# Kernel tuning notes

Measured on AMD Instinct MI355X. Metric: run time of the kernel, lower is better.

Reference implementation:

```python
import jax, jax.numpy as jnp
import numpy as np

NUM_CLASSES = 80
BATCH_PER_IMG = 512
POS_FRAC = 0.25
IOU_THRESH = 0.5
NUM_FG_TARGET = int(BATCH_PER_IMG * POS_FRAC)  # 128


def _make_boxes(k, shape):
    raw = jax.random.uniform(k, shape + (4,), dtype=jnp.float32)
    x1 = raw[..., 0] * 900.0
    y1 = raw[..., 1] * 900.0
    w = raw[..., 2] * 120.0 + 4.0
    h = raw[..., 3] * 120.0 + 4.0
    return jnp.stack([x1, y1, x1 + w, y1 + h], axis=-1)


def setup_inputs() -> dict:
    B, N, M = 16, 20000, 128
    key = jax.random.key(0)
    k1, k2, k3, k4, k5 = jax.random.split(key, 5)
    gt_boxes = _make_boxes(k1, (B, M))
    proposal_boxes = _make_boxes(k2, (B, N))
    # make the first M proposals jittered copies of gt so some match above IoU 0.5
    jitter = jax.random.normal(k5, (B, M, 4), dtype=jnp.float32) * 3.0
    proposal_boxes = proposal_boxes.at[:, :M, :].set(gt_boxes + jitter)
    gt_classes = jax.random.randint(k3, (B, M), 0, NUM_CLASSES)
    keys = jax.random.uniform(k4, (B, N), dtype=jnp.float32)  # random sampling priorities
    return {"gt_boxes": gt_boxes, "gt_classes": gt_classes,
            "proposal_boxes": proposal_boxes, "keys": keys}


def _pairwise_iou(gt, pr):
    # gt: [M,4], pr: [N,4], xyxy -> [M,N]
    area_g = (gt[:, 2] - gt[:, 0]) * (gt[:, 3] - gt[:, 1])
    area_p = (pr[:, 2] - pr[:, 0]) * (pr[:, 3] - pr[:, 1])
    lt = jnp.maximum(gt[:, None, :2], pr[None, :, :2])
    rb = jnp.minimum(gt[:, None, 2:], pr[None, :, 2:])
    wh = jnp.clip(rb - lt, 0.0)
    inter = wh[..., 0] * wh[..., 1]
    return inter / (area_g[:, None] + area_p[None, :] - inter)


def _per_image(gt_b, gt_c, pr_b, key_f):
    iou = _pairwise_iou(gt_b, pr_b)          # [M,N]
    matched_vals = iou.max(axis=0)           # [N]  (ious in torch code)
    matched_idxs = iou.argmax(axis=0)        # [N]  matcher assignment
    matched_labels = matched_vals >= IOU_THRESH  # thresholds [0.5], labels [0,1]
    cls = jnp.where(matched_labels, gt_c[matched_idxs], NUM_CLASSES)  # bg = num_classes
    fg = cls != NUM_CLASSES
    fg_take = jnp.minimum(NUM_FG_TARGET, fg.sum())  # subsample_labels fg quota
    BIG = jnp.float32(1e9)
    fg_order = jnp.argsort(jnp.where(fg, key_f, BIG))   # random fg subset via random keys
    bg_order = jnp.argsort(jnp.where(fg, BIG, key_f))   # random bg subset
    i = jnp.arange(BATCH_PER_IMG)
    sampled = jnp.where(i < fg_take, fg_order[i], bg_order[jnp.clip(i - fg_take, 0)])
    s_cls = cls[sampled]                         # gt_classes field
    s_iou = matched_vals[sampled]                # proposals.iou field
    s_gt_boxes = gt_b[matched_idxs[sampled]]     # gt_boxes field gather
    float_out = jnp.concatenate([s_iou[:, None], s_gt_boxes], axis=-1)  # [512,5]
    return sampled, s_cls, float_out


def reference(gt_boxes, gt_classes, proposal_boxes, keys):
    sampled_idxs, sampled_classes, float_out = jax.vmap(_per_image)(
        gt_boxes, gt_classes, proposal_boxes, keys)
    return float_out, sampled_classes, sampled_idxs
```

## Files before the change

### kernel.cpp

```cpp
#include <hip/hip_runtime.h>
#include <stdint.h>

constexpr int Bn     = 16;
constexpr int Nn     = 20000;
constexpr int Mn     = 128;
constexpr int NCLS   = 80;
constexpr int BATCH  = 512;
constexpr int FG_TGT = 128;
constexpr float KEY_T = 0.06f;

constexpr int TPB = 256;
constexpr int TPI = (Nn + TPB - 1) / TPB;
constexpr int NT  = Bn * TPI;

typedef unsigned long long u64;

__global__ __launch_bounds__(256) void classify_kernel(
    const float* __restrict__ gt_boxes, const float* __restrict__ prop,
    const float* __restrict__ keys,
    u64* __restrict__ fgsl, u64* __restrict__ bgsl,
    int* __restrict__ fcnt, int* __restrict__ bcnt)
{
    const int t    = blockIdx.x;
    const int b    = t / TPI;
    const int blk  = t % TPI;
    const int tid  = threadIdx.x;
    const int lane = tid & 63;

    __shared__ u64 fgl[256];
    __shared__ u64 bgl[256];
    __shared__ int lcnt[2];
    if (tid < 2) lcnt[tid] = 0;
    __syncthreads();

    const float4 g0 = ((const float4*)gt_boxes)[(size_t)b * Mn + 2 * lane];
    const float4 g1 = ((const float4*)gt_boxes)[(size_t)b * Mn + 2 * lane + 1];
    const float a0 = __fmul_rn(__fsub_rn(g0.z, g0.x), __fsub_rn(g0.w, g0.y));
    const float a1 = __fmul_rn(__fsub_rn(g1.z, g1.x), __fsub_rn(g1.w, g1.y));

    const int n0 = __builtin_amdgcn_readfirstlane(blk * 256 + (tid >> 6) * 64);
    const float4* __restrict__ pp = (const float4*)prop + (size_t)b * Nn + n0;
    u64 fgmask = 0;

#define IOU_BODY(IDX)                                                          \
    {                                                                          \
        const float4 p = pp[IDX];                       \
        const float ap = __fmul_rn(__fsub_rn(p.z, p.x), __fsub_rn(p.w, p.y)); \
        float w0 = fmaxf(__fsub_rn(fminf(g0.z, p.z), fmaxf(g0.x, p.x)), 0.0f);\
        float h0 = fmaxf(__fsub_rn(fminf(g0.w, p.w), fmaxf(g0.y, p.y)), 0.0f);\
        float i0 = __fmul_rn(w0, h0);                                          \
        float d0 = __fsub_rn(__fadd_rn(a0, ap), i0);                           \
        float q0 = __fadd_rn(i0, i0);                                          \
        float t0 = __builtin_fmaf(d0, -0x1p-20f, d0);                          \
        float w1 = fmaxf(__fsub_rn(fminf(g1.z, p.z), fmaxf(g1.x, p.x)), 0.0f);\
        float h1 = fmaxf(__fsub_rn(fminf(g1.w, p.w), fmaxf(g1.y, p.y)), 0.0f);\
        float i1 = __fmul_rn(w1, h1);                                          \
        float d1 = __fsub_rn(__fadd_rn(a1, ap), i1);                           \
        float q1 = __fadd_rn(i1, i1);                                          \
        float t1 = __builtin_fmaf(d1, -0x1p-20f, d1);                          \
        bool ambl = (q0 >= t0) | (q1 >= t1);                                   \
        if (__ballot(ambl) != 0) {                     \
            bool e0 = (2.0 * (double)i0 >= (double)d0 * (1.0 - 0x1p-25));      \
            bool e1 = (2.0 * (double)i1 >= (double)d1 * (1.0 - 0x1p-25));      \
            bool def = __ballot(e0 | e1) != 0;                                 \
            fgmask |= ((u64)(def ? 1 : 0)) << (IDX);                           \
        }                                                                      \
    }

    if (n0 + 64 <= Nn) {
        #pragma unroll 8
        for (int i = 0; i < 64; ++i) IOU_BODY(i)
    } else if (n0 < Nn) {
        const int lim = Nn - n0;
        for (int i = 0; i < lim; ++i) IOU_BODY(i)
    }
#undef IOU_BODY

    const int  nl  = n0 + lane;
    const bool okl = (n0 < Nn) && (nl < Nn);
    const float k  = okl ? keys[(size_t)b * Nn + nl] : 1.0f;
    const bool fg  = okl && (((fgmask >> lane) & 1ull) != 0);
    const bool bgp = okl && !fg && (k < KEY_T);
    const u64 comp = ((u64)__float_as_uint(k) << 32) | (unsigned)nl;

    {
        u64 m = __ballot(fg);
        if (m) {
            int leader = __ffsll((unsigned long long)m) - 1;
            int base = 0;
            if (lane == leader) base = atomicAdd(&lcnt[0], (int)__popcll(m));
            base = __shfl(base, leader, 64);
            if (fg) fgl[base + (int)__popcll(m & ((1ull << lane) - 1))] = comp;
        }
        m = __ballot(bgp);
        if (m) {
            int leader = __ffsll((unsigned long long)m) - 1;
            int base = 0;
            if (lane == leader) base = atomicAdd(&lcnt[1], (int)__popcll(m));
            base = __shfl(base, leader, 64);
            if (bgp) bgl[base + (int)__popcll(m & ((1ull << lane) - 1))] = comp;
        }
    }
    __syncthreads();

    u64* __restrict__ F = fgsl + (size_t)t * 256;
    u64* __restrict__ G = bgsl + (size_t)t * 256;
    for (int j = tid; j < lcnt[0]; j += 256) F[j] = fgl[j];
    for (int j = tid; j < lcnt[1]; j += 256) G[j] = bgl[j];
    if (tid == 0)  fcnt[t] = lcnt[0];
    if (tid == 64) bcnt[t] = lcnt[1];
}

constexpr int SPLIT = 32;
constexpr int NCF   = 16;
constexpr int NCB   = 24;
constexpr int FSLOT = 8;
constexpr int BSLOT = 12;

__device__ __forceinline__ int wave_incl_scan(int v, int lane)
{
    #pragma unroll
    for (int off = 1; off < 64; off <<= 1) {
        int n = __shfl_up(v, off, 64);
        if (lane >= off) v += n;
    }
    return v;
}

__global__ __launch_bounds__(256) void select_finalize_kernel(
    const float* __restrict__ gt_boxes, const int* __restrict__ gt_classes,
    const float* __restrict__ prop,
    const u64* __restrict__ fgsl, const u64* __restrict__ bgsl,
    const int* __restrict__ fcnt, const int* __restrict__ bcnt,
    float* __restrict__ out)
{
    const int b    = blockIdx.x / SPLIT;
    const int sb   = blockIdx.x % SPLIT;
    const int tid  = threadIdx.x;
    const int wv   = tid >> 6;
    const int lane = tid & 63;
    const int wimg = sb * 4 + wv;
    const int hw   = wimg >> 6;
    const int wl   = wimg & 63;

    __shared__ u64 D[NCB * 64];
    __shared__ int pfx[TPI + 1];
    __shared__ int rowbuf[128];
    __shared__ int ecnt;
    if (tid == 0) ecnt = 0;

    float* idx_out = out + (size_t)Bn * BATCH * 5 + (size_t)Bn * BATCH;

    if (wv == 0) {
        int a  = fcnt[b * TPI + lane];
        int b2 = (lane < TPI - 64) ? fcnt[b * TPI + 64 + lane] : 0;
        int sa  = wave_incl_scan(a, lane);
        int ta  = __shfl(sa, 63, 64);
        int sb2 = wave_incl_scan(b2, lane) + ta;
        if (lane == 0) pfx[0] = 0;
        pfx[1 + lane] = sa;
        if (lane < TPI - 64) pfx[65 + lane] = sb2;
    }
    __syncthreads();
    const int nf      = pfx[TPI];
    const int nfc     = min(nf, NCF * 64);
    const int fg_take = min(FG_TGT, nf);
    const int bg_need = BATCH - fg_take;

    for (int i = tid; i < nfc; i += 256) {
        int lo = 0, hi = TPI;
        #pragma unroll
        for (int it = 0; it < 7; ++it) { int mid = (lo + hi) >> 1; if (pfx[mid] <= i) lo = mid; else hi = mid; }
        D[i] = fgsl[((size_t)(b * TPI + lo)) * 256 + (i - pfx[lo])];
    }
    __syncthreads();
    {
        u64 S[NCF];
        #pragma unroll
        for (int c = 0; c < NCF; ++c) {
            int p2 = c * 64 + lane;
            S[c] = (p2 < nfc) ? D[p2] : ~0ull;
        }
        #pragma unroll
        for (int s = 0; s < FSLOT; ++s) {
            int j = wimg + 128 * s;
            if (j >= nfc) break;
            u64 me = __shfl(hw ? S[2 * s + 1] : S[2 * s], wl, 64);
            int r = 0;
            #pragma unroll
            for (int c = 0; c < NCF; ++c)
                r += (int)__popcll(__ballot(S[c] < me));
            if (r < fg_take && lane == 0) {
                int idx = (int)(me & 0xffffffffu);
                idx_out[b * BATCH + r] = (float)idx;
                int e = atomicAdd(&ecnt, 1);
                rowbuf[e] = (r << 16) | idx;
            }
        }
    }
    __syncthreads();

    if (wv == 0) {
        int a  = bcnt[b * TPI + lane];
        int b2 = (lane < TPI - 64) ? bcnt[b * TPI + 64 + lane] : 0;
        int sa  = wave_incl_scan(a, lane);
        int ta  = __shfl(sa, 63, 64);
        int sb2 = wave_incl_scan(b2, lane) + ta;
        if (lane == 0) pfx[0] = 0;
        pfx[1 + lane] = sa;
        if (lane < TPI - 64) pfx[65 + lane] = sb2;
    }
    __syncthreads();
    const int nb  = pfx[TPI];
    const int nbc = min(nb, NCB * 64);

    for (int i = tid; i < nbc; i += 256) {
        int lo = 0, hi = TPI;
        #pragma unroll
        for (int it = 0; it < 7; ++it) { int mid = (lo + hi) >> 1; if (pfx[mid] <= i) lo = mid; else hi = mid; }
        D[i] = bgsl[((size_t)(b * TPI + lo)) * 256 + (i - pfx[lo])];
    }
    __syncthreads();
    {
        u64 S[NCB];
        #pragma unroll
        for (int c = 0; c < NCB; ++c) {
            int p2 = c * 64 + lane;
            S[c] = (p2 < nbc) ? D[p2] : ~0ull;
        }
        #pragma unroll
        for (int s = 0; s < BSLOT; ++s) {
            int j = wimg + 128 * s;
            if (j >= nbc) break;
            u64 me = __shfl(hw ? S[2 * s + 1] : S[2 * s], wl, 64);
            int r = 0;
            #pragma unroll
            for (int c = 0; c < NCB; ++c)
                r += (int)__popcll(__ballot(S[c] < me));
            if (r < bg_need && lane == 0) {
                int idx = (int)(me & 0xffffffffu);
                int row = fg_take + r;
                idx_out[b * BATCH + row] = (float)idx;
                int e = atomicAdd(&ecnt, 1);
                rowbuf[e] = (row << 16) | idx;
            }
        }
    }
    __syncthreads();

    const int ne = ecnt;
    for (int e = wv; e < ne; e += 4) {
        const int packed = rowbuf[e];
        const int row = packed >> 16, idx = packed & 0xffff;
        const float4 p  = ((const float4*)prop)[(size_t)b * Nn + idx];
        const float  ap = __fmul_rn(__fsub_rn(p.z, p.x), __fsub_rn(p.w, p.y));
        u64 best = 0;
        #pragma unroll
        for (int half = 0; half < 2; ++half) {
            const int m = lane + 64 * half;
            float4 g    = ((const float4*)gt_boxes)[(size_t)b * Mn + m];
            float ag    = __fmul_rn(__fsub_rn(g.z, g.x), __fsub_rn(g.w, g.y));
            float w     = fmaxf(__fsub_rn(fminf(g.z, p.z), fmaxf(g.x, p.x)), 0.0f);
            float h     = fmaxf(__fsub_rn(fminf(g.w, p.w), fmaxf(g.y, p.y)), 0.0f);
            float inter = __fmul_rn(w, h);
            float den   = __fsub_rn(__fadd_rn(ag, ap), inter);
            float v     = __fdiv_rn(inter, den);
            u64 key = ((u64)__float_as_uint(v) << 32) | (unsigned)(Mn - 1 - m);
            best = key > best ? key : best;
        }
        #pragma unroll
        for (int off = 1; off < 64; off <<= 1) {
            u64 o = (u64)__shfl_xor((unsigned long long)best, off, 64);
            best = o > best ? o : best;
        }
        const float v  = __uint_as_float((unsigned)(best >> 32));
        const int   mi = Mn - 1 - (int)(best & 0xffffffffu);
        const float4 gg = ((const float4*)gt_boxes)[(size_t)b * Mn + mi];
        if (lane < 5) {
            float w5 = (lane == 0) ? v
                     : (lane == 1) ? gg.x
                     : (lane == 2) ? gg.y
                     : (lane == 3) ? gg.z : gg.w;
            out[((size_t)(b * BATCH + row)) * 5 + lane] = w5;
        }
        if (lane == 5) {
            int cls = (v >= 0.5f) ? gt_classes[b * Mn + mi] : NCLS;
            out[(size_t)Bn * BATCH * 5 + b * BATCH + row] = (float)cls;
        }
    }
}

extern "C" void kernel_launch(void* const* d_in, const int* in_sizes, int n_in,
                              void* d_out, int out_size, void* d_ws, size_t ws_size,
                              hipStream_t stream)
{
    const float* gt_boxes   = (const float*)d_in[0];
    const int*   gt_classes = (const int*)  d_in[1];
    const float* prop       = (const float*)d_in[2];
    const float* keys       = (const float*)d_in[3];
    float*       out        = (float*)d_out;

    char* ws   = (char*)d_ws;
    u64*  fgsl = (u64*)ws;
    u64*  bgsl = (u64*)(ws + (size_t)NT * 256 * 8);
    int*  fcnt = (int*)(ws + (size_t)NT * 256 * 16);
    int*  bcnt = (int*)(ws + (size_t)NT * 256 * 16 + NT * 4);

    classify_kernel<<<NT, 256, 0, stream>>>(gt_boxes, prop, keys,
                                            fgsl, bgsl, fcnt, bcnt);
    select_finalize_kernel<<<Bn * SPLIT, 256, 0, stream>>>(gt_boxes, gt_classes,
                                                           prop, fgsl, bgsl,
                                                           fcnt, bcnt, out);
}
```

Before: 107.3 us.

## Prefilter gt candidates by center containment before exact IoU check

Replaces the per-wave lane-per-gt IoU sweep over 64 proposals with a one-thread-per-proposal scheme. Each thread tests which gt centers fall inside its slightly enlarged proposal box, building a bitmask, then computes the exact IoU only for those candidates. The reasoning is that IoU >= 0.5 between two axis-aligned boxes implies each box contains the other's center. This cuts most of the M×N IoU arithmetic, at the cost of divergent while-loops over candidate bits and gt boxes staged in shared memory.

```diff
diff --git a/kernel.cpp b/kernel.cpp
--- a/kernel.cpp
+++ b/kernel.cpp
@@ -1,5 +1,7 @@
 #include <hip/hip_runtime.h>
 #include <stdint.h>
+
+typedef unsigned long long u64;
 
 constexpr int Bn     = 16;
 constexpr int Nn     = 20000;
@@ -13,7 +15,35 @@
 constexpr int TPI = (Nn + TPB - 1) / TPB;
 constexpr int NT  = Bn * TPI;
 
-typedef unsigned long long u64;
+constexpr float EPS = 0.0625f;
+
+
+__device__ __forceinline__ bool resolve_exact(const float4* gbox, const float4 P,
+                                              const float ap,
+                                              unsigned m0, unsigned m1,
+                                              unsigned m2, unsigned m3)
+{
+    bool fg = false;
+    unsigned bw[4] = {m0, m1, m2, m3};
+    #pragma unroll
+    for (int c = 0; c < 4; ++c) {
+        unsigned bits = bw[c];
+        while (__ballot(bits != 0) != 0) {
+            if (bits) {
+                const int k = __ffs(bits) - 1;
+                bits &= bits - 1;
+                const float4 g = gbox[32 * c + k];
+                const float ag = __fmul_rn(__fsub_rn(g.z, g.x), __fsub_rn(g.w, g.y));
+                const float w  = fmaxf(__fsub_rn(fminf(g.z, P.z), fmaxf(g.x, P.x)), 0.0f);
+                const float h  = fmaxf(__fsub_rn(fminf(g.w, P.w), fmaxf(g.y, P.y)), 0.0f);
+                const float it = __fmul_rn(w, h);
+                const float dn = __fsub_rn(__fadd_rn(ag, ap), it);
+                if (2.0 * (double)it >= (double)dn * (1.0 - 0x1p-25)) fg = true;
+            }
+        }
+    }
+    return fg;
+}
 
 __global__ __launch_bounds__(256) void classify_kernel(
     const float* __restrict__ gt_boxes, const float* __restrict__ prop,
@@ -27,66 +57,58 @@
     const int tid  = threadIdx.x;
     const int lane = tid & 63;
 
-    __shared__ u64 fgl[256];
-    __shared__ u64 bgl[256];
-    __shared__ int lcnt[2];
+    __shared__ float4 gbox[Mn];
+    __shared__ float4 gctr4[Mn / 2];
+    __shared__ u64    fgl[TPB];
+    __shared__ u64    bgl[TPB];
+    __shared__ int    lcnt[2];
     if (tid < 2) lcnt[tid] = 0;
-    __syncthreads();
-
-    const float4 g0 = ((const float4*)gt_boxes)[(size_t)b * Mn + 2 * lane];
-    const float4 g1 = ((const float4*)gt_boxes)[(size_t)b * Mn + 2 * lane + 1];
-    const float a0 = __fmul_rn(__fsub_rn(g0.z, g0.x), __fsub_rn(g0.w, g0.y));
-    const float a1 = __fmul_rn(__fsub_rn(g1.z, g1.x), __fsub_rn(g1.w, g1.y));
-
-    const int n0 = __builtin_amdgcn_readfirstlane(blk * 256 + (tid >> 6) * 64);
-    const float4* __restrict__ pp = (const float4*)prop + (size_t)b * Nn + n0;
-    u64 fgmask = 0;
-
-#define IOU_BODY(IDX)                                                          \
-    {                                                                          \
-        const float4 p = pp[IDX];                       \
-        const float ap = __fmul_rn(__fsub_rn(p.z, p.x), __fsub_rn(p.w, p.y)); \
-        float w0 = fmaxf(__fsub_rn(fminf(g0.z, p.z), fmaxf(g0.x, p.x)), 0.0f);\
-        float h0 = fmaxf(__fsub_rn(fminf(g0.w, p.w), fmaxf(g0.y, p.y)), 0.0f);\
-        float i0 = __fmul_rn(w0, h0);                                          \
-        float d0 = __fsub_rn(__fadd_rn(a0, ap), i0);                           \
-        float q0 = __fadd_rn(i0, i0);                                          \
-        float t0 = __builtin_fmaf(d0, -0x1p-20f, d0);                          \
-        float w1 = fmaxf(__fsub_rn(fminf(g1.z, p.z), fmaxf(g1.x, p.x)), 0.0f);\
-        float h1 = fmaxf(__fsub_rn(fminf(g1.w, p.w), fmaxf(g1.y, p.y)), 0.0f);\
-        float i1 = __fmul_rn(w1, h1);                                          \
-        float d1 = __fsub_rn(__fadd_rn(a1, ap), i1);                           \
-        float q1 = __fadd_rn(i1, i1);                                          \
-        float t1 = __builtin_fmaf(d1, -0x1p-20f, d1);                          \
-        bool ambl = (q0 >= t0) | (q1 >= t1);                                   \
-        if (__ballot(ambl) != 0) {                     \
-            bool e0 = (2.0 * (double)i0 >= (double)d0 * (1.0 - 0x1p-25));      \
-            bool e1 = (2.0 * (double)i1 >= (double)d1 * (1.0 - 0x1p-25));      \
-            bool def = __ballot(e0 | e1) != 0;                                 \
-            fgmask |= ((u64)(def ? 1 : 0)) << (IDX);                           \
-        }                                                                      \
-    }
-
-    if (n0 + 64 <= Nn) {
-        #pragma unroll 8
-        for (int i = 0; i < 64; ++i) IOU_BODY(i)
-    } else if (n0 < Nn) {
-        const int lim = Nn - n0;
-        for (int i = 0; i < lim; ++i) IOU_BODY(i)
-    }
-#undef IOU_BODY
-
-    const int  nl  = n0 + lane;
-    const bool okl = (n0 < Nn) && (nl < Nn);
-    const float k  = okl ? keys[(size_t)b * Nn + nl] : 1.0f;
-    const bool fg  = okl && (((fgmask >> lane) & 1ull) != 0);
-    const bool bgp = okl && !fg && (k < KEY_T);
-    const u64 comp = ((u64)__float_as_uint(k) << 32) | (unsigned)nl;
-
+
+    for (int m = tid; m < Mn; m += 256)
+        gbox[m] = ((const float4*)gt_boxes)[(size_t)b * Mn + m];
+    if (tid < Mn / 2) {
+        const float4 ga = ((const float4*)gt_boxes)[(size_t)b * Mn + 2 * tid];
+        const float4 gb = ((const float4*)gt_boxes)[(size_t)b * Mn + 2 * tid + 1];
+        gctr4[tid] = make_float4(0.5f * __fadd_rn(ga.x, ga.z),
+                                 0.5f * __fadd_rn(ga.y, ga.w),
+                                 0.5f * __fadd_rn(gb.x, gb.z),
+                                 0.5f * __fadd_rn(gb.y, gb.w));
+    }
+
+    const int  n  = blk * TPB + tid;
+    const bool ok = (n < Nn);
+    const float4 P = ((const float4*)prop)[(size_t)b * Nn + (ok ? n : 0)];
+    const float x1e = P.x - EPS, x2e = P.z + EPS;
+    const float y1e = P.y - EPS, y2e = P.w + EPS;
+    const float ap  = __fmul_rn(__fsub_rn(P.z, P.x), __fsub_rn(P.w, P.y));
+    __syncthreads();
+
+    unsigned acc[4];
+    #pragma unroll
+    for (int c = 0; c < 4; ++c) {
+        unsigned A = 0;
+        #pragma unroll 4
+        for (int j = 15; j >= 0; --j) {
+            const float4 cc = gctr4[16 * c + j];
+            const unsigned p0 = (unsigned)((x1e <= cc.x) & (cc.x <= x2e) &
+                                           (y1e <= cc.y) & (cc.y <= y2e));
+            const unsigned p1 = (unsigned)((x1e <= cc.z) & (cc.z <= x2e) &
+                                           (y1e <= cc.w) & (cc.w <= y2e));
+            A = (A << 2) | (p1 << 1) | p0;
+        }
+        acc[c] = A;
+    }
+
+    const bool fgr = resolve_exact(gbox, P, ap, acc[0], acc[1], acc[2], acc[3]);
+
+    const float k  = ok ? keys[(size_t)b * Nn + n] : 1.0f;
+    const bool fg  = ok && fgr;
+    const bool bgp = ok && !fg && (k < KEY_T);
+    const u64 comp = ((u64)__float_as_uint(k) << 32) | (unsigned)n;
     {
         u64 m = __ballot(fg);
         if (m) {
-            int leader = __ffsll((unsigned long long)m) - 1;
+            const int leader = __ffsll((unsigned long long)m) - 1;
             int base = 0;
             if (lane == leader) base = atomicAdd(&lcnt[0], (int)__popcll(m));
             base = __shfl(base, leader, 64);
@@ -94,7 +116,7 @@
         }
         m = __ballot(bgp);
         if (m) {
-            int leader = __ffsll((unsigned long long)m) - 1;
+            const int leader = __ffsll((unsigned long long)m) - 1;
             int base = 0;
             if (lane == leader) base = atomicAdd(&lcnt[1], (int)__popcll(m));
             base = __shfl(base, leader, 64);
```

Measured after the change: 96.41 us. 1.11x faster.
